# Optimization experiments

Measured on AMD Instinct MI355X. Metric: run time of the kernel, lower is better.

The kernel has to match this reference:

```python
import jax, jax.numpy as jnp
import numpy as np

B, C, H, W = 16, 256, 128, 128  # H must equal W for this module's dilation trick to be consistent
K = 2  # kernel_size (lifting taps)


def setup_inputs() -> dict:
    key = jax.random.key(0)
    ks = jax.random.split(key, 6)
    C4 = C // 4
    return {
        "x": jax.random.normal(ks[0], (B, C, H, W), jnp.float32),
        "conv1x1_w": jax.random.normal(ks[1], (C, C), jnp.float32) / np.sqrt(C).astype(np.float32),
        "lp_v": jax.random.uniform(ks[2], (C4, 1, K, 1), jnp.float32),  # low_pass_filter_v
        "hp_v": jax.random.uniform(ks[3], (C4, 1, K, 1), jnp.float32),  # high_pass_filter_v
        "lp_h": jax.random.uniform(ks[4], (C4, 1, 1, K), jnp.float32),  # low_pass_filter_h
        "hp_h": jax.random.uniform(ks[5], (C4, 1, 1, K), jnp.float32),  # high_pass_filter_h
    }


def _interleave(e, o, axis):
    # interleave e/o along `axis`: out[..., 2i, ...] = e[..., i, ...], out[..., 2i+1, ...] = o[..., i, ...]
    s = jnp.stack([e, o], axis=axis + 1)
    sh = list(e.shape)
    sh[axis] *= 2
    return s.reshape(sh)


def reference(x, conv1x1_w, lp_v, hp_v, lp_h, hp_h):
    # 1x1 conv (no bias)
    x = jnp.einsum('bchw,oc->bohw', x, conv1x1_w)
    b_, c_, h_, w_ = x.shape
    # pad_mode == 'discard': crop to multiple of kernel_size
    x = x[:, :, :h_ - h_ % K, :w_ - w_ % K]
    c4 = c_ // 4
    a = x[:, :c4]
    bq = x[:, c4:2 * c4]
    cq = x[:, 2 * c4:3 * c4]
    dq = x[:, 3 * c4:]
    # per-channel 2-tap combos: w0 * first_half + w1 * second_half
    lv0 = lp_v[:, 0, 0, 0][None, :, None, None]; lv1 = lp_v[:, 0, 1, 0][None, :, None, None]
    hv0 = hp_v[:, 0, 0, 0][None, :, None, None]; hv1 = hp_v[:, 0, 1, 0][None, :, None, None]
    lh0 = lp_h[:, 0, 0, 0][None, :, None, None]; lh1 = lp_h[:, 0, 0, 1][None, :, None, None]
    hh0 = hp_h[:, 0, 0, 0][None, :, None, None]; hh1 = hp_h[:, 0, 0, 1][None, :, None, None]
    # vertical lifting + row interleave -> [B, C/4, 2H, W]
    x_l = _interleave(lv0 * a + lv1 * bq, hv0 * a + hv1 * bq, 2)
    x_h = _interleave(lv0 * cq + lv1 * dq, hv0 * cq + hv1 * dq, 2)
    # horizontal lifting (valid because H == W) + column interleave -> [B, C/4, 2H, 2W]
    x_e = lh0 * x_l + lh1 * x_h
    x_o = hh0 * x_l + hh1 * x_h
    return _interleave(x_e, x_o, 3)
```

## Files before the change

kernel.cpp:

```cpp
#include <hip/hip_runtime.h>

#define HW 16384

typedef __attribute__((ext_vector_type(8))) __bf16 bf16x8;
typedef __attribute__((ext_vector_type(16))) float floatx16;
typedef __attribute__((ext_vector_type(8))) unsigned short ushort8_t;

typedef const __attribute__((address_space(1))) unsigned int gu32;
typedef __attribute__((address_space(3))) unsigned int lu32;

__device__ __forceinline__ unsigned short f2bf(float f) {
    unsigned int u = __builtin_bit_cast(unsigned int, f);
    unsigned int r = (u + 0x7FFFu + ((u >> 16) & 1u)) >> 16;
    return (unsigned short)r;
}

__device__ __forceinline__ void gload_lds16(const unsigned short* g, unsigned short* l) {
    __builtin_amdgcn_global_load_lds((gu32*)g, (lu32*)l, 16, 0, 0);
}

__global__ void wconv_kernel(const float* __restrict__ w, unsigned short* __restrict__ wb) {
    int i = blockIdx.x * 256 + threadIdx.x;
    int row = i >> 8, c = i & 255;
    int kt = c >> 6, kl = c & 63;
    int idx = (row * 64 + kl) ^ ((row & 7) << 3);
    wb[kt * 16384 + idx] = f2bf(w[i]);
}

__global__ __launch_bounds__(512, 2) void fused_gemm_lift(
        const float* __restrict__ x,
        const unsigned short* __restrict__ wb,
        const float* __restrict__ lp_v,
        const float* __restrict__ hp_v,
        const float* __restrict__ lp_h,
        const float* __restrict__ hp_h,
        float* __restrict__ out) {
    __shared__ alignas(16) unsigned short wbuf_s[4][16384];

    const int tid  = threadIdx.x;
    const int wv   = tid >> 6;
    const int lane = tid & 63;
    const int l31  = lane & 31;
    const int chunk = lane >> 5;
    const int tile = blockIdx.x & 63;
    const int bb   = blockIdx.x >> 6;
    const int p0   = tile * 256;

    const float* xp = x + (size_t)bb * 256 * HW + p0 + wv * 32 + l31;

    floatx16 acc[8];
    #pragma unroll
    for (int mt = 0; mt < 8; ++mt)
        #pragma unroll
        for (int e = 0; e < 16; ++e) acc[mt][e] = 0.f;

    float xf[2][32];

    #pragma unroll
    for (int jj = 0; jj < 32; ++jj) {
        int c = (jj >> 3) * 16 + chunk * 8 + (jj & 7);
        xf[0][jj] = xp[(size_t)c * HW];
    }
    #pragma unroll
    for (int p = 0; p < 16; ++p)
        gload_lds16(wb + (size_t)(p * 512 + tid) * 8, &wbuf_s[0][0] + (size_t)(p * 512 + tid) * 8);
    __syncthreads();

    #pragma unroll
    for (int kt = 0; kt < 4; ++kt) {
        const int cw = kt & 1;

        if (kt < 3) {
            #pragma unroll
            for (int jj = 0; jj < 32; ++jj) {
                int c = (kt + 1) * 64 + (jj >> 3) * 16 + chunk * 8 + (jj & 7);
                xf[cw ^ 1][jj] = xp[(size_t)c * HW];
            }
        }

        #pragma unroll
        for (int k16 = 0; k16 < 4; ++k16) {
            ushort8_t u;
            #pragma unroll
            for (int j = 0; j < 8; ++j) u[j] = f2bf(xf[cw][k16 * 8 + j]);
            const bf16x8 bq = __builtin_bit_cast(bf16x8, u);
            const int kl = k16 * 16 + chunk * 8;
            #pragma unroll
            for (int mt = 0; mt < 8; ++mt) {
                const int row = mt * 32 + l31;
                bf16x8 af = *reinterpret_cast<const bf16x8*>(
                    &wbuf_s[kt][(row * 64 + kl) ^ ((row & 7) << 3)]);
                acc[mt] = __builtin_amdgcn_mfma_f32_32x32x16_bf16(af, bq, acc[mt], 0, 0, 0);
            }
        }
    }

    const int px = p0 + wv * 32 + l31;
    const int h  = px >> 7;
    const int w  = px & 127;
    float* outbase = out + (size_t)bb * 64 * 65536 + (size_t)(2 * h) * 256 + 2 * w;
    const int hi = lane >> 5;
    #pragma unroll
    for (int mt2 = 0; mt2 < 2; ++mt2)
        #pragma unroll
        for (int reg = 0; reg < 16; ++reg) {
            const int row = (reg & 3) + 8 * (reg >> 2) + 4 * hi;
            const int q = mt2 * 32 + row;
            const float2 lv = *reinterpret_cast<const float2*>(lp_v + 2 * q);
            const float2 hv = *reinterpret_cast<const float2*>(hp_v + 2 * q);
            const float2 lh = *reinterpret_cast<const float2*>(lp_h + 2 * q);
            const float2 hh = *reinterpret_cast<const float2*>(hp_h + 2 * q);
            const float a  = acc[mt2][reg];
            const float b2 = acc[mt2 + 2][reg];
            const float c2 = acc[mt2 + 4][reg];
            const float d2 = acc[mt2 + 6][reg];
            const float xl0 = lv.x * a + lv.y * b2;
            const float xl1 = hv.x * a + hv.y * b2;
            const float xh0 = lv.x * c2 + lv.y * d2;
            const float xh1 = hv.x * c2 + hv.y * d2;
            float2 r0 = make_float2(lh.x * xl0 + lh.y * xh0, hh.x * xl0 + hh.y * xh0);
            float2 r1 = make_float2(lh.x * xl1 + lh.y * xh1, hh.x * xl1 + hh.y * xh1);
            float* oq = outbase + (size_t)q * 65536;
            *reinterpret_cast<float2*>(oq)       = r0;
            *reinterpret_cast<float2*>(oq + 256) = r1;
        }
}

extern "C" void kernel_launch(void* const* d_in, const int* in_sizes, int n_in,
                              void* d_out, int out_size, void* d_ws, size_t ws_size,
                              hipStream_t stream) {
    const float* x   = (const float*)d_in[0];
    const float* w   = (const float*)d_in[1];
    const float* lpv = (const float*)d_in[2];
    const float* hpv = (const float*)d_in[3];
    const float* lph = (const float*)d_in[4];
    const float* hph = (const float*)d_in[5];
    float* outp = (float*)d_out;
    unsigned short* wbp = (unsigned short*)d_ws;

    wconv_kernel<<<dim3(256), dim3(256), 0, stream>>>(w, wbp);
    fused_gemm_lift<<<dim3(1024), dim3(512), 0, stream>>>(x, wbp, lpv, hpv, lph, hph, outp);
}
```

Before: 136.3 us.

## Halve pixel tile, split M across wave pairs, double-buffer weight LDS

Each block now covers 128 pixels instead of 256, and pairs of waves split the 256 output rows, so each wave holds 4 accumulator tiles instead of 8. Weights are streamed into a two-slot LDS double buffer per K-chunk rather than loaded all at once. Activation prefetch is split into half-chunks, and barriers use explicit vmcnt waits. The aim is to cut LDS and register use so four blocks fit per CU, hiding memory latency. The cost is that each x element is loaded by two waves and each block does more weight loads and barriers.

```diff
diff --git a/kernel.cpp b/kernel.cpp
--- a/kernel.cpp
+++ b/kernel.cpp
@@ -27,7 +27,7 @@
     wb[kt * 16384 + idx] = f2bf(w[i]);
 }
 
-__global__ __launch_bounds__(512, 2) void fused_gemm_lift(
+__global__ __launch_bounds__(512, 4) void fused_gemm_lift(
         const float* __restrict__ x,
         const unsigned short* __restrict__ wb,
         const float* __restrict__ lp_v,
@@ -35,36 +35,42 @@
         const float* __restrict__ lp_h,
         const float* __restrict__ hp_h,
         float* __restrict__ out) {
-    __shared__ alignas(16) unsigned short wbuf_s[4][16384];
+    __shared__ alignas(16) unsigned short wbuf_s[2][16384];
 
     const int tid  = threadIdx.x;
     const int wv   = tid >> 6;
     const int lane = tid & 63;
-    const int l31  = lane & 31;
-    const int chunk = lane >> 5;
-    const int tile = blockIdx.x & 63;
-    const int bb   = blockIdx.x >> 6;
-    const int p0   = tile * 256;
+    const int pw   = wv >> 1;
+    const int sub  = wv & 1;
+    const int tile = blockIdx.x & 127;
+    const int bb   = blockIdx.x >> 7;
+    const int p0   = tile * 128;
 
-    const float* xp = x + (size_t)bb * 256 * HW + p0 + wv * 32 + l31;
+    const int l31 = lane & 31;
+    const int hi  = lane >> 5;
 
-    floatx16 acc[8];
+    const float* xp = x + (size_t)bb * 256 * HW + p0 + pw * 32 + l31;
+
+    floatx16 acc[4];
     #pragma unroll
-    for (int mt = 0; mt < 8; ++mt)
+    for (int j4 = 0; j4 < 4; ++j4)
         #pragma unroll
-        for (int e = 0; e < 16; ++e) acc[mt][e] = 0.f;
+        for (int e = 0; e < 16; ++e) acc[j4][e] = 0.f;
 
-    float xf[2][32];
+    float xf0[16], xf1[16];
 
     #pragma unroll
-    for (int jj = 0; jj < 32; ++jj) {
-        int c = (jj >> 3) * 16 + chunk * 8 + (jj & 7);
-        xf[0][jj] = xp[(size_t)c * HW];
-    }
+    for (int p = 0; p < 4; ++p)
+        gload_lds16(wb + (size_t)(p * 512 + tid) * 8, &wbuf_s[0][(p * 512 + tid) * 8]);
     #pragma unroll
-    for (int p = 0; p < 16; ++p)
-        gload_lds16(wb + (size_t)(p * 512 + tid) * 8, &wbuf_s[0][0] + (size_t)(p * 512 + tid) * 8);
-    __syncthreads();
+    for (int k16 = 0; k16 < 2; ++k16)
+        #pragma unroll
+        for (int j = 0; j < 8; ++j)
+            xf0[k16 * 8 + j] = xp[(size_t)(k16 * 16 + hi * 8 + j) * HW];
+    asm volatile("s_waitcnt vmcnt(16)" ::: "memory");
+    __builtin_amdgcn_sched_barrier(0);
+    __builtin_amdgcn_s_barrier();
+    __builtin_amdgcn_sched_barrier(0);
 
     #pragma unroll
     for (int kt = 0; kt < 4; ++kt) {
@@ -72,58 +78,95 @@
 
         if (kt < 3) {
             #pragma unroll
-            for (int jj = 0; jj < 32; ++jj) {
-                int c = (kt + 1) * 64 + (jj >> 3) * 16 + chunk * 8 + (jj & 7);
-                xf[cw ^ 1][jj] = xp[(size_t)c * HW];
+            for (int p = 0; p < 4; ++p)
+                gload_lds16(wb + (size_t)(kt + 1) * 16384 + (size_t)(p * 512 + tid) * 8,
+                            &wbuf_s[cw ^ 1][(p * 512 + tid) * 8]);
+        }
+
+        {
+            const int cb = kt * 64 + 32;
+            #pragma unroll
+            for (int k16 = 0; k16 < 2; ++k16)
+                #pragma unroll
+                for (int j = 0; j < 8; ++j)
+                    xf1[k16 * 8 + j] = xp[(size_t)(cb + k16 * 16 + hi * 8 + j) * HW];
+        }
+
+        #pragma unroll
+        for (int k16 = 0; k16 < 2; ++k16) {
+            ushort8_t u;
+            #pragma unroll
+            for (int j = 0; j < 8; ++j) u[j] = f2bf(xf0[k16 * 8 + j]);
+            const bf16x8 bq = __builtin_bit_cast(bf16x8, u);
+            const int kl = k16 * 16 + hi * 8;
+            #pragma unroll
+            for (int j4 = 0; j4 < 4; ++j4) {
+                const int row = (2 * j4 + sub) * 32 + l31;
+                bf16x8 af = *reinterpret_cast<const bf16x8*>(
+                    &wbuf_s[cw][(row * 64 + kl) ^ ((row & 7) << 3)]);
+                acc[j4] = __builtin_amdgcn_mfma_f32_32x32x16_bf16(af, bq, acc[j4], 0, 0, 0);
             }
         }
 
+        if (kt < 3) {
+            const int cb = kt * 64 + 64;
+            #pragma unroll
+            for (int k16 = 0; k16 < 2; ++k16)
+                #pragma unroll
+                for (int j = 0; j < 8; ++j)
+                    xf0[k16 * 8 + j] = xp[(size_t)(cb + k16 * 16 + hi * 8 + j) * HW];
+        }
+
         #pragma unroll
-        for (int k16 = 0; k16 < 4; ++k16) {
+        for (int k16 = 0; k16 < 2; ++k16) {
             ushort8_t u;
             #pragma unroll
-            for (int j = 0; j < 8; ++j) u[j] = f2bf(xf[cw][k16 * 8 + j]);
+            for (int j = 0; j < 8; ++j) u[j] = f2bf(xf1[k16 * 8 + j]);
             const bf16x8 bq = __builtin_bit_cast(bf16x8, u);
-            const int kl = k16 * 16 + chunk * 8;
+            const int kl = 32 + k16 * 16 + hi * 8;
             #pragma unroll
-            for (int mt = 0; mt < 8; ++mt) {
-                const int row = mt * 32 + l31;
+            for (int j4 = 0; j4 < 4; ++j4) {
+                const int row = (2 * j4 + sub) * 32 + l31;
                 bf16x8 af = *reinterpret_cast<const bf16x8*>(
-                    &wbuf_s[kt][(row * 64 + kl) ^ ((row & 7) << 3)]);
-                acc[mt] = __builtin_amdgcn_mfma_f32_32x32x16_bf16(af, bq, acc[mt], 0, 0, 0);
+                    &wbuf_s[cw][(row * 64 + kl) ^ ((row & 7) << 3)]);
+                acc[j4] = __builtin_amdgcn_mfma_f32_32x32x16_bf16(af, bq, acc[j4], 0, 0, 0);
             }
+        }
+
+        if (kt < 3) {
+            asm volatile("s_waitcnt vmcnt(16)" ::: "memory");
+            __builtin_amdgcn_sched_barrier(0);
+            __builtin_amdgcn_s_barrier();
+            __builtin_amdgcn_sched_barrier(0);
         }
     }
 
-    const int px = p0 + wv * 32 + l31;
+    const int px = p0 + pw * 32 + l31;
     const int h  = px >> 7;
     const int w  = px & 127;
     float* outbase = out + (size_t)bb * 64 * 65536 + (size_t)(2 * h) * 256 + 2 * w;
-    const int hi = lane >> 5;
     #pragma unroll
-    for (int mt2 = 0; mt2 < 2; ++mt2)
-        #pragma unroll
-        for (int reg = 0; reg < 16; ++reg) {
-            const int row = (reg & 3) + 8 * (reg >> 2) + 4 * hi;
-            const int q = mt2 * 32 + row;
-            const float2 lv = *reinterpret_cast<const float2*>(lp_v + 2 * q);
-            const float2 hv = *reinterpret_cast<const float2*>(hp_v + 2 * q);
-            const float2 lh = *reinterpret_cast<const float2*>(lp_h + 2 * q);
-            const float2 hh = *reinterpret_cast<const float2*>(hp_h + 2 * q);
-            const float a  = acc[mt2][reg];
-            const float b2 = acc[mt2 + 2][reg];
-            const float c2 = acc[mt2 + 4][reg];
-            const float d2 = acc[mt2 + 6][reg];
-            const float xl0 = lv.x * a + lv.y * b2;
-            const float xl1 = hv.x * a + hv.y * b2;
-            const float xh0 = lv.x * c2 + lv.y * d2;
-            const float xh1 = hv.x * c2 + hv.y * d2;
-            float2 r0 = make_float2(lh.x * xl0 + lh.y * xh0, hh.x * xl0 + hh.y * xh0);
-            float2 r1 = make_float2(lh.x * xl1 + lh.y * xh1, hh.x * xl1 + hh.y * xh1);
-            float* oq = outbase + (size_t)q * 65536;
-            *reinterpret_cast<float2*>(oq)       = r0;
-            *reinterpret_cast<float2*>(oq + 256) = r1;
-        }
+    for (int reg = 0; reg < 16; ++reg) {
+        const int rowl = (reg & 3) + 8 * (reg >> 2) + 4 * hi;
+        const int q = sub * 32 + rowl;
+        const float2 lv = *reinterpret_cast<const float2*>(lp_v + 2 * q);
+        const float2 hv = *reinterpret_cast<const float2*>(hp_v + 2 * q);
+        const float2 lh = *reinterpret_cast<const float2*>(lp_h + 2 * q);
+        const float2 hh = *reinterpret_cast<const float2*>(hp_h + 2 * q);
+        const float a  = acc[0][reg];
+        const float b2 = acc[1][reg];
+        const float c2 = acc[2][reg];
+        const float d2 = acc[3][reg];
+        const float xl0 = lv.x * a + lv.y * b2;
+        const float xl1 = hv.x * a + hv.y * b2;
+        const float xh0 = lv.x * c2 + lv.y * d2;
+        const float xh1 = hv.x * c2 + hv.y * d2;
+        float2 r0 = make_float2(lh.x * xl0 + lh.y * xh0, hh.x * xl0 + hh.y * xh0);
+        float2 r1 = make_float2(lh.x * xl1 + lh.y * xh1, hh.x * xl1 + hh.y * xh1);
+        float* oq = outbase + (size_t)q * 65536;
+        *reinterpret_cast<float2*>(oq)       = r0;
+        *reinterpret_cast<float2*>(oq + 256) = r1;
+    }
 }
 
 extern "C" void kernel_launch(void* const* d_in, const int* in_sizes, int n_in,
@@ -139,5 +182,5 @@
     unsigned short* wbp = (unsigned short*)d_ws;
 
     wconv_kernel<<<dim3(256), dim3(256), 0, stream>>>(w, wbp);
-    fused_gemm_lift<<<dim3(1024), dim3(512), 0, stream>>>(x, wbp, lpv, hpv, lph, hph, outp);
+    fused_gemm_lift<<<dim3(2048), dim3(512), 0, stream>>>(x, wbp, lpv, hpv, lph, hph, outp);
 }
```

Result: slower. 401.9 us (+194.8%).

## Stage x and weights through double-buffered LDS and coalesce output via LDS

Applied to the files above, without the earlier changes.

Halves the pixel tile to 128 per block and doubles the grid. Each wave pair now splits the output channels. Both x and the bf16 weights are staged into double-buffered LDS with direct global-to-LDS loads, using explicit vmcnt waits and barriers so loads overlap the MFMA work. Output is written to an LDS chunk first and then stored as coalesced float4 rows, replacing the strided float2 stores. This uses 128KB of LDS per block, which likely limits occupancy to one block per CU, and adds extra barriers.

```diff
diff --git a/kernel.cpp b/kernel.cpp
--- a/kernel.cpp
+++ b/kernel.cpp
@@ -15,7 +15,7 @@
     return (unsigned short)r;
 }
 
-__device__ __forceinline__ void gload_lds16(const unsigned short* g, unsigned short* l) {
+__device__ __forceinline__ void gload_lds16(const void* g, void* l) {
     __builtin_amdgcn_global_load_lds((gu32*)g, (lu32*)l, 16, 0, 0);
 }
 
@@ -35,95 +35,147 @@
         const float* __restrict__ lp_h,
         const float* __restrict__ hp_h,
         float* __restrict__ out) {
-    __shared__ alignas(16) unsigned short wbuf_s[4][16384];
+    __shared__ alignas(16) unsigned char smem[131072];
+
+    float* xb0 = (float*)smem;
+    float* xb1 = (float*)(smem + 32768);
+    unsigned short* wbb0 = (unsigned short*)(smem + 65536);
+    unsigned short* wbb1 = (unsigned short*)(smem + 98304);
 
     const int tid  = threadIdx.x;
     const int wv   = tid >> 6;
     const int lane = tid & 63;
-    const int l31  = lane & 31;
-    const int chunk = lane >> 5;
-    const int tile = blockIdx.x & 63;
-    const int bb   = blockIdx.x >> 6;
-    const int p0   = tile * 256;
+    const int pw   = wv >> 1;
+    const int sub  = wv & 1;
+    const int t    = blockIdx.x & 127;
+    const int bb   = blockIdx.x >> 7;
+    const int p0   = t * 128;
 
-    const float* xp = x + (size_t)bb * 256 * HW + p0 + wv * 32 + l31;
+    const int l31 = lane & 31;
+    const int hi  = lane >> 5;
+    const int px  = pw * 32 + l31;
 
-    floatx16 acc[8];
+    const float* xg = x + (size_t)bb * 256 * HW + p0;
+
+    floatx16 acc[4];
     #pragma unroll
-    for (int mt = 0; mt < 8; ++mt)
+    for (int j4 = 0; j4 < 4; ++j4)
         #pragma unroll
-        for (int e = 0; e < 16; ++e) acc[mt][e] = 0.f;
+        for (int e = 0; e < 16; ++e) acc[j4][e] = 0.f;
 
-    float xf[2][32];
+    #define STAGE_X(KT, BUF) do {                                              \
+        _Pragma("unroll")                                                      \
+        for (int i_ = 0; i_ < 4; ++i_) {                                       \
+            int g_ = i_ * 512 + tid;                                           \
+            int c_ = (KT) * 64 + (g_ >> 5);                                    \
+            int o_ = (g_ & 31) * 4;                                            \
+            gload_lds16(xg + (size_t)c_ * HW + o_, (char*)(BUF) + g_ * 16);    \
+        } } while (0)
 
-    #pragma unroll
-    for (int jj = 0; jj < 32; ++jj) {
-        int c = (jj >> 3) * 16 + chunk * 8 + (jj & 7);
-        xf[0][jj] = xp[(size_t)c * HW];
-    }
-    #pragma unroll
-    for (int p = 0; p < 16; ++p)
-        gload_lds16(wb + (size_t)(p * 512 + tid) * 8, &wbuf_s[0][0] + (size_t)(p * 512 + tid) * 8);
+    #define STAGE_W(KT, BUF) do {                                              \
+        _Pragma("unroll")                                                      \
+        for (int p_ = 0; p_ < 4; ++p_) {                                       \
+            int idx_ = p_ * 512 + tid;                                         \
+            gload_lds16(wb + (size_t)(KT) * 16384 + (size_t)idx_ * 8,          \
+                        (char*)(BUF) + idx_ * 16);                             \
+        } } while (0)
+
+    #define COMPUTE(XBF, WBF) do {                                             \
+        _Pragma("unroll")                                                      \
+        for (int k16_ = 0; k16_ < 4; ++k16_) {                                 \
+            const int kl_ = k16_ * 16 + hi * 8;                                \
+            float xv_[8];                                                      \
+            _Pragma("unroll")                                                  \
+            for (int j_ = 0; j_ < 8; ++j_)                                     \
+                xv_[j_] = (XBF)[(kl_ + j_) * 128 + px];                        \
+            ushort8_t u_;                                                      \
+            _Pragma("unroll")                                                  \
+            for (int j_ = 0; j_ < 8; ++j_) u_[j_] = f2bf(xv_[j_]);             \
+            const bf16x8 bq_ = __builtin_bit_cast(bf16x8, u_);                 \
+            _Pragma("unroll")                                                  \
+            for (int j4_ = 0; j4_ < 4; ++j4_) {                                \
+                const int row_ = (2 * j4_ + sub) * 32 + l31;                   \
+                bf16x8 af_ = *reinterpret_cast<const bf16x8*>(                 \
+                    &(WBF)[(row_ * 64 + kl_) ^ ((row_ & 7) << 3)]);            \
+                acc[j4_] = __builtin_amdgcn_mfma_f32_32x32x16_bf16(            \
+                    af_, bq_, acc[j4_], 0, 0, 0);                              \
+            }                                                                  \
+        } } while (0)
+
+    STAGE_X(0, xb0);
+    STAGE_W(0, wbb0);
+    STAGE_X(1, xb1);
+    asm volatile("s_waitcnt vmcnt(4)" ::: "memory");
+    __builtin_amdgcn_s_barrier();
+
+    STAGE_W(1, wbb1);
+    COMPUTE(xb0, wbb0);
+    __builtin_amdgcn_s_barrier();
+    STAGE_X(2, xb0);
+    asm volatile("s_waitcnt vmcnt(4)" ::: "memory");
+    __builtin_amdgcn_s_barrier();
+
+    STAGE_W(2, wbb0);
+    COMPUTE(xb1, wbb1);
+    __builtin_amdgcn_s_barrier();
+    STAGE_X(3, xb1);
+    asm volatile("s_waitcnt vmcnt(4)" ::: "memory");
+    __builtin_amdgcn_s_barrier();
+
+    STAGE_W(3, wbb1);
+    COMPUTE(xb0, wbb0);
+    __builtin_amdgcn_s_barrier();
+    asm volatile("s_waitcnt vmcnt(0)" ::: "memory");
+    __builtin_amdgcn_s_barrier();
+
+    COMPUTE(xb1, wbb1);
     __syncthreads();
 
+    float* chunk = (float*)smem;
     #pragma unroll
-    for (int kt = 0; kt < 4; ++kt) {
-        const int cw = kt & 1;
-
-        if (kt < 3) {
+    for (int qc = 0; qc < 2; ++qc) {
+        if (sub == qc) {
             #pragma unroll
-            for (int jj = 0; jj < 32; ++jj) {
-                int c = (kt + 1) * 64 + (jj >> 3) * 16 + chunk * 8 + (jj & 7);
-                xf[cw ^ 1][jj] = xp[(size_t)c * HW];
+            for (int reg = 0; reg < 16; ++reg) {
+                const int rowl = (reg & 3) + 8 * (reg >> 2) + 4 * hi;
+                const int q = sub * 32 + rowl;
+                const float2 lv = *reinterpret_cast<const float2*>(lp_v + 2 * q);
+                const float2 hv = *reinterpret_cast<const float2*>(hp_v + 2 * q);
+                const float2 lh = *reinterpret_cast<const float2*>(lp_h + 2 * q);
+                const float2 hh = *reinterpret_cast<const float2*>(hp_h + 2 * q);
+                const float a  = acc[0][reg];
+                const float b2 = acc[1][reg];
+                const float c2 = acc[2][reg];
+                const float d2 = acc[3][reg];
+                const float xl0 = lv.x * a + lv.y * b2;
+                const float xl1 = hv.x * a + hv.y * b2;
+                const float xh0 = lv.x * c2 + lv.y * d2;
+                const float xh1 = hv.x * c2 + hv.y * d2;
+                float2 r0 = make_float2(lh.x * xl0 + lh.y * xh0, hh.x * xl0 + hh.y * xh0);
+                float2 r1 = make_float2(lh.x * xl1 + lh.y * xh1, hh.x * xl1 + hh.y * xh1);
+                *reinterpret_cast<float2*>(&chunk[(rowl * 2 + 0) * 256 + 2 * px]) = r0;
+                *reinterpret_cast<float2*>(&chunk[(rowl * 2 + 1) * 256 + 2 * px]) = r1;
             }
         }
-
+        __syncthreads();
         #pragma unroll
-        for (int k16 = 0; k16 < 4; ++k16) {
-            ushort8_t u;
-            #pragma unroll
-            for (int j = 0; j < 8; ++j) u[j] = f2bf(xf[cw][k16 * 8 + j]);
-            const bf16x8 bq = __builtin_bit_cast(bf16x8, u);
-            const int kl = k16 * 16 + chunk * 8;
-            #pragma unroll
-            for (int mt = 0; mt < 8; ++mt) {
-                const int row = mt * 32 + l31;
-                bf16x8 af = *reinterpret_cast<const bf16x8*>(
-                    &wbuf_s[kt][(row * 64 + kl) ^ ((row & 7) << 3)]);
-                acc[mt] = __builtin_amdgcn_mfma_f32_32x32x16_bf16(af, bq, acc[mt], 0, 0, 0);
-            }
+        for (int i = 0; i < 8; ++i) {
+            const int g = i * 512 + tid;
+            const int rowid = g >> 6;
+            const int qloc  = rowid >> 1;
+            const int r     = rowid & 1;
+            const int col   = (g & 63) * 4;
+            float4 v = reinterpret_cast<const float4*>(chunk)[g];
+            *reinterpret_cast<float4*>(
+                out + (size_t)(bb * 64 + qc * 32 + qloc) * 65536
+                    + (size_t)(2 * t + r) * 256 + col) = v;
         }
+        __syncthreads();
     }
 
-    const int px = p0 + wv * 32 + l31;
-    const int h  = px >> 7;
-    const int w  = px & 127;
-    float* outbase = out + (size_t)bb * 64 * 65536 + (size_t)(2 * h) * 256 + 2 * w;
-    const int hi = lane >> 5;
-    #pragma unroll
-    for (int mt2 = 0; mt2 < 2; ++mt2)
-        #pragma unroll
-        for (int reg = 0; reg < 16; ++reg) {
-            const int row = (reg & 3) + 8 * (reg >> 2) + 4 * hi;
-            const int q = mt2 * 32 + row;
-            const float2 lv = *reinterpret_cast<const float2*>(lp_v + 2 * q);
-            const float2 hv = *reinterpret_cast<const float2*>(hp_v + 2 * q);
-            const float2 lh = *reinterpret_cast<const float2*>(lp_h + 2 * q);
-            const float2 hh = *reinterpret_cast<const float2*>(hp_h + 2 * q);
-            const float a  = acc[mt2][reg];
-            const float b2 = acc[mt2 + 2][reg];
-            const float c2 = acc[mt2 + 4][reg];
-            const float d2 = acc[mt2 + 6][reg];
-            const float xl0 = lv.x * a + lv.y * b2;
-            const float xl1 = hv.x * a + hv.y * b2;
-            const float xh0 = lv.x * c2 + lv.y * d2;
-            const float xh1 = hv.x * c2 + hv.y * d2;
-            float2 r0 = make_float2(lh.x * xl0 + lh.y * xh0, hh.x * xl0 + hh.y * xh0);
-            float2 r1 = make_float2(lh.x * xl1 + lh.y * xh1, hh.x * xl1 + hh.y * xh1);
-            float* oq = outbase + (size_t)q * 65536;
-            *reinterpret_cast<float2*>(oq)       = r0;
-            *reinterpret_cast<float2*>(oq + 256) = r1;
-        }
+    #undef STAGE_X
+    #undef STAGE_W
+    #undef COMPUTE
 }
 
 extern "C" void kernel_launch(void* const* d_in, const int* in_sizes, int n_in,
@@ -139,5 +191,5 @@
     unsigned short* wbp = (unsigned short*)d_ws;
 
     wconv_kernel<<<dim3(256), dim3(256), 0, stream>>>(w, wbp);
-    fused_gemm_lift<<<dim3(1024), dim3(512), 0, stream>>>(x, wbp, lpv, hpv, lph, hph, outp);
+    fused_gemm_lift<<<dim3(2048), dim3(512), 0, stream>>>(x, wbp, lpv, hpv, lph, hph, outp);
 }
```

After: 137.9 us. About the same (+1.1%).

## Split output channels across two blocks to halve LDS and accumulators

Applied to the files above, without the earlier changes.

Each block now computes half of the output-channel quads (32 of each 64-channel group), so the weight slice in LDS drops from 128KB to 64KB and accumulators from 8 to 4 MFMA tiles. The grid doubles and launch bounds request 4 blocks per CU, with x prefetch double-buffered in 32-channel phases instead of 64. The intent is higher occupancy to hide global-load latency. In exchange, every x element is read and converted to bf16 twice, once by each of the two blocks.

```diff
diff --git a/kernel.cpp b/kernel.cpp
--- a/kernel.cpp
+++ b/kernel.cpp
@@ -15,7 +15,7 @@
     return (unsigned short)r;
 }
 
-__device__ __forceinline__ void gload_lds16(const unsigned short* g, unsigned short* l) {
+__device__ __forceinline__ void gload_lds16(const void* g, void* l) {
     __builtin_amdgcn_global_load_lds((gu32*)g, (lu32*)l, 16, 0, 0);
 }
 
@@ -27,7 +27,7 @@
     wb[kt * 16384 + idx] = f2bf(w[i]);
 }
 
-__global__ __launch_bounds__(512, 2) void fused_gemm_lift(
+__global__ __launch_bounds__(512, 4) void fused_gemm_lift(
         const float* __restrict__ x,
         const unsigned short* __restrict__ wb,
         const float* __restrict__ lp_v,
@@ -35,95 +35,109 @@
         const float* __restrict__ lp_h,
         const float* __restrict__ hp_h,
         float* __restrict__ out) {
-    __shared__ alignas(16) unsigned short wbuf_s[4][16384];
+    __shared__ alignas(16) unsigned short wlds[32768];
 
     const int tid  = threadIdx.x;
     const int wv   = tid >> 6;
     const int lane = tid & 63;
     const int l31  = lane & 31;
-    const int chunk = lane >> 5;
-    const int tile = blockIdx.x & 63;
-    const int bb   = blockIdx.x >> 6;
-    const int p0   = tile * 256;
+    const int hi   = lane >> 5;
 
-    const float* xp = x + (size_t)bb * 256 * HW + p0 + wv * 32 + l31;
+    const int qb = blockIdx.x & 1;
+    const int pt = (blockIdx.x >> 1) & 63;
+    const int bb = blockIdx.x >> 7;
 
-    floatx16 acc[8];
-    #pragma unroll
-    for (int mt = 0; mt < 8; ++mt)
-        #pragma unroll
-        for (int e = 0; e < 16; ++e) acc[mt][e] = 0.f;
-
-    float xf[2][32];
+    const int px = pt * 256 + wv * 32 + l31;
+    const float* xp = x + (size_t)bb * 256 * HW + px;
 
     #pragma unroll
-    for (int jj = 0; jj < 32; ++jj) {
-        int c = (jj >> 3) * 16 + chunk * 8 + (jj & 7);
-        xf[0][jj] = xp[(size_t)c * HW];
+    for (int it = 0; it < 8; ++it) {
+        const int f  = it * 512 + tid;
+        const int rs = (f >> 3) & 127;
+        const int kt = f >> 10;
+        const int pc = f & 7;
+        const int grow = (rs & 31) + qb * 32 + (rs >> 5) * 64;
+        gload_lds16(wb + (size_t)kt * 16384 + grow * 64 + pc * 8,
+                    (char*)wlds + (size_t)f * 16);
     }
-    #pragma unroll
-    for (int p = 0; p < 16; ++p)
-        gload_lds16(wb + (size_t)(p * 512 + tid) * 8, &wbuf_s[0][0] + (size_t)(p * 512 + tid) * 8);
     __syncthreads();
 
+    floatx16 acc[4];
     #pragma unroll
-    for (int kt = 0; kt < 4; ++kt) {
-        const int cw = kt & 1;
+    for (int g = 0; g < 4; ++g)
+        #pragma unroll
+        for (int e = 0; e < 16; ++e) acc[g][e] = 0.f;
 
-        if (kt < 3) {
-            #pragma unroll
-            for (int jj = 0; jj < 32; ++jj) {
-                int c = (kt + 1) * 64 + (jj >> 3) * 16 + chunk * 8 + (jj & 7);
-                xf[cw ^ 1][jj] = xp[(size_t)c * HW];
-            }
-        }
+    float xf0[16], xf1[16];
 
-        #pragma unroll
-        for (int k16 = 0; k16 < 4; ++k16) {
-            ushort8_t u;
-            #pragma unroll
-            for (int j = 0; j < 8; ++j) u[j] = f2bf(xf[cw][k16 * 8 + j]);
-            const bf16x8 bq = __builtin_bit_cast(bf16x8, u);
-            const int kl = k16 * 16 + chunk * 8;
-            #pragma unroll
-            for (int mt = 0; mt < 8; ++mt) {
-                const int row = mt * 32 + l31;
-                bf16x8 af = *reinterpret_cast<const bf16x8*>(
-                    &wbuf_s[kt][(row * 64 + kl) ^ ((row & 7) << 3)]);
-                acc[mt] = __builtin_amdgcn_mfma_f32_32x32x16_bf16(af, bq, acc[mt], 0, 0, 0);
-            }
-        }
+    #pragma unroll
+    for (int j = 0; j < 16; ++j) {
+        const int c = (j >> 3) * 16 + hi * 8 + (j & 7);
+        xf0[j] = xp[(size_t)c * HW];
     }
 
-    const int px = p0 + wv * 32 + l31;
-    const int h  = px >> 7;
-    const int w  = px & 127;
+    #define PHASE(PH, CUR, NXT) do {                                           \
+        if ((PH) < 7) {                                                        \
+            _Pragma("unroll")                                                  \
+            for (int j_ = 0; j_ < 16; ++j_) {                                  \
+                const int c_ = ((PH) + 1) * 32 + (j_ >> 3) * 16 + hi * 8 + (j_ & 7); \
+                NXT[j_] = xp[(size_t)c_ * HW];                                 \
+            }                                                                  \
+        }                                                                      \
+        _Pragma("unroll")                                                      \
+        for (int s_ = 0; s_ < 2; ++s_) {                                       \
+            ushort8_t u_;                                                      \
+            _Pragma("unroll")                                                  \
+            for (int j_ = 0; j_ < 8; ++j_) u_[j_] = f2bf(CUR[s_ * 8 + j_]);    \
+            const bf16x8 bq_ = __builtin_bit_cast(bf16x8, u_);                 \
+            const int k16_ = 2 * (PH) + s_;                                    \
+            const int kt_  = k16_ >> 2;                                        \
+            const int kl_  = (k16_ & 3) * 16 + hi * 8;                         \
+            _Pragma("unroll")                                                  \
+            for (int g_ = 0; g_ < 4; ++g_) {                                   \
+                const int rs_ = g_ * 32 + l31;                                 \
+                bf16x8 af_ = *reinterpret_cast<const bf16x8*>(                 \
+                    &wlds[kt_ * 8192 + rs_ * 64 + (kl_ ^ ((rs_ & 7) << 3))]);  \
+                acc[g_] = __builtin_amdgcn_mfma_f32_32x32x16_bf16(             \
+                    af_, bq_, acc[g_], 0, 0, 0);                               \
+            }                                                                  \
+        } } while (0)
+
+    PHASE(0, xf0, xf1);
+    PHASE(1, xf1, xf0);
+    PHASE(2, xf0, xf1);
+    PHASE(3, xf1, xf0);
+    PHASE(4, xf0, xf1);
+    PHASE(5, xf1, xf0);
+    PHASE(6, xf0, xf1);
+    PHASE(7, xf1, xf0);
+    #undef PHASE
+
+    const int h = px >> 7;
+    const int w = px & 127;
     float* outbase = out + (size_t)bb * 64 * 65536 + (size_t)(2 * h) * 256 + 2 * w;
-    const int hi = lane >> 5;
     #pragma unroll
-    for (int mt2 = 0; mt2 < 2; ++mt2)
-        #pragma unroll
-        for (int reg = 0; reg < 16; ++reg) {
-            const int row = (reg & 3) + 8 * (reg >> 2) + 4 * hi;
-            const int q = mt2 * 32 + row;
-            const float2 lv = *reinterpret_cast<const float2*>(lp_v + 2 * q);
-            const float2 hv = *reinterpret_cast<const float2*>(hp_v + 2 * q);
-            const float2 lh = *reinterpret_cast<const float2*>(lp_h + 2 * q);
-            const float2 hh = *reinterpret_cast<const float2*>(hp_h + 2 * q);
-            const float a  = acc[mt2][reg];
-            const float b2 = acc[mt2 + 2][reg];
-            const float c2 = acc[mt2 + 4][reg];
-            const float d2 = acc[mt2 + 6][reg];
-            const float xl0 = lv.x * a + lv.y * b2;
-            const float xl1 = hv.x * a + hv.y * b2;
-            const float xh0 = lv.x * c2 + lv.y * d2;
-            const float xh1 = hv.x * c2 + hv.y * d2;
-            float2 r0 = make_float2(lh.x * xl0 + lh.y * xh0, hh.x * xl0 + hh.y * xh0);
-            float2 r1 = make_float2(lh.x * xl1 + lh.y * xh1, hh.x * xl1 + hh.y * xh1);
-            float* oq = outbase + (size_t)q * 65536;
-            *reinterpret_cast<float2*>(oq)       = r0;
-            *reinterpret_cast<float2*>(oq + 256) = r1;
-        }
+    for (int reg = 0; reg < 16; ++reg) {
+        const int rowl = (reg & 3) + 8 * (reg >> 2) + 4 * hi;
+        const int q = qb * 32 + rowl;
+        const float2 lv = *reinterpret_cast<const float2*>(lp_v + 2 * q);
+        const float2 hv = *reinterpret_cast<const float2*>(hp_v + 2 * q);
+        const float2 lh = *reinterpret_cast<const float2*>(lp_h + 2 * q);
+        const float2 hh = *reinterpret_cast<const float2*>(hp_h + 2 * q);
+        const float a  = acc[0][reg];
+        const float b2 = acc[1][reg];
+        const float c2 = acc[2][reg];
+        const float d2 = acc[3][reg];
+        const float xl0 = lv.x * a + lv.y * b2;
+        const float xl1 = hv.x * a + hv.y * b2;
+        const float xh0 = lv.x * c2 + lv.y * d2;
+        const float xh1 = hv.x * c2 + hv.y * d2;
+        float2 r0 = make_float2(lh.x * xl0 + lh.y * xh0, hh.x * xl0 + hh.y * xh0);
+        float2 r1 = make_float2(lh.x * xl1 + lh.y * xh1, hh.x * xl1 + hh.y * xh1);
+        float* oq = outbase + (size_t)q * 65536;
+        *reinterpret_cast<float2*>(oq)       = r0;
+        *reinterpret_cast<float2*>(oq + 256) = r1;
+    }
 }
 
 extern "C" void kernel_launch(void* const* d_in, const int* in_sizes, int n_in,
@@ -139,5 +153,5 @@
     unsigned short* wbp = (unsigned short*)d_ws;
 
     wconv_kernel<<<dim3(256), dim3(256), 0, stream>>>(w, wbp);
-    fused_gemm_lift<<<dim3(1024), dim3(512), 0, stream>>>(x, wbp, lpv, hpv, lph, hph, outp);
+    fused_gemm_lift<<<dim3(2048), dim3(512), 0, stream>>>(x, wbp, lpv, hpv, lph, hph, outp);
 }
```

New measurement: 143.9 us. 5.5% more time.
